# Kernel optimization log

Measured on AMD Instinct MI355X. Metric: run time of the kernel, lower is better.

## Reference

```python
import jax, jax.numpy as jnp
import numpy as np

B, S, E, H = 8, 1025, 1408, 16
D = E // H  # 88 head_dim


def setup_inputs() -> dict:
    key = jax.random.key(0)
    ks = jax.random.split(key, 12)
    w_scale = 0.02
    hidden_states = jax.random.normal(ks[0], (B, S, E), dtype=jnp.float32)
    ang = jax.random.uniform(ks[1], (S, D // 2), dtype=jnp.float32) * (2.0 * np.pi)
    freqs_cos = jnp.cos(ang)
    freqs_sin = jnp.sin(ang)
    Wq = jax.random.normal(ks[2], (E, E), dtype=jnp.float32) * w_scale
    bq = jax.random.normal(ks[3], (E,), dtype=jnp.float32) * w_scale
    Wk = jax.random.normal(ks[4], (E, E), dtype=jnp.float32) * w_scale
    bk = jax.random.normal(ks[5], (E,), dtype=jnp.float32) * w_scale
    Wv = jax.random.normal(ks[6], (E, E), dtype=jnp.float32) * w_scale
    bv = jax.random.normal(ks[7], (E,), dtype=jnp.float32) * w_scale
    Wo = jax.random.normal(ks[8], (E, E), dtype=jnp.float32) * w_scale
    bo = jax.random.normal(ks[9], (E,), dtype=jnp.float32) * w_scale
    return {"hidden_states": hidden_states, "freqs_cos": freqs_cos, "freqs_sin": freqs_sin,
            "Wq": Wq, "bq": bq, "Wk": Wk, "bk": bk, "Wv": Wv, "bv": bv, "Wo": Wo, "bo": bo}


def _apply_rope(x, cos, sin):
    # x: (B,S,H,D); interpret last dim as D/2 complex pairs (real, imag)
    xr = x[..., 0::2]  # (B,S,H,D/2) -- pairs laid out interleaved after reshape(..., -1, 2)
    xi = x[..., 1::2]
    c = cos[None, :, None, :]  # (1,S,1,D/2)
    s = sin[None, :, None, :]
    or_ = xr * c - xi * s
    oi_ = xr * s + xi * c
    # interleave back: (..., D/2, 2) -> (..., D)
    return jnp.stack([or_, oi_], axis=-1).reshape(x.shape)


def reference(hidden_states, freqs_cos, freqs_sin, Wq, bq, Wk, bk, Wv, bv, Wo, bo):
    b, s, e = hidden_states.shape
    h, d = H, D
    q = (hidden_states @ Wq.T + bq).reshape(b, s, h, d)
    k = (hidden_states @ Wk.T + bk).reshape(b, s, h, d)
    v = (hidden_states @ Wv.T + bv).reshape(b, s, h, d)
    q = _apply_rope(q, freqs_cos, freqs_sin)
    k = _apply_rope(k, freqs_cos, freqs_sin)
    scale = d ** (-0.5)
    # (B,H,S,S) attention scores; no mask, non-causal, dropout=0 (eval)
    scores = jnp.einsum("bshd,bthd->bhst", q, k) * scale
    w = jax.nn.softmax(scores, axis=-1)
    out = jnp.einsum("bhst,bthd->bshd", w, v).reshape(b, s, e)
    return out @ Wo.T + bo
```

## Files before the change

kernel.cpp:

```cpp
#include <hip/hip_runtime.h>
#include <stdint.h>
#include <stddef.h>

#define Bsz 8
#define Ssz 1025
#define Esz 1408
#define Hsz 16
#define Dsz 88
#define Msz (Bsz * Ssz)
#define HALF_E (Esz / 2)
#define HALF_D (Dsz / 2)
#define SPAD 1088
#define QSC 0.15379182f

typedef __attribute__((ext_vector_type(8))) short short8;
typedef __attribute__((ext_vector_type(4))) float f32x4;

__device__ __forceinline__ unsigned short f2bf(float f) {
  union { float f; unsigned u; } v; v.f = f;
  unsigned r = v.u + 0x7fffu + ((v.u >> 16) & 1u);
  return (unsigned short)(r >> 16);
}
__device__ __forceinline__ unsigned fbits(float f) {
  union { float f; unsigned u; } v; v.f = f; return v.u;
}
__device__ __forceinline__ float fexp2(float x) {
#if __has_builtin(__builtin_amdgcn_exp2f)
  return __builtin_amdgcn_exp2f(x);
#else
  return __expf(x * 0.6931471805599453f);
#endif
}

__global__ void cast_kernel(const float* __restrict__ in, unsigned short* __restrict__ out, int n4) {
  int i = blockIdx.x * blockDim.x + threadIdx.x;
  if (i >= n4) return;
  float4 v = ((const float4*)in)[i];
  uint2 o;
  o.x = (unsigned)f2bf(v.x) | ((unsigned)f2bf(v.y) << 16);
  o.y = (unsigned)f2bf(v.z) | ((unsigned)f2bf(v.w) << 16);
  ((uint2*)out)[i] = o;
}

__global__ void cast4_kernel(const float* __restrict__ a, const float* __restrict__ b,
                             const float* __restrict__ c, const float* __restrict__ d,
                             unsigned short* __restrict__ out, int n4each) {
  int i = blockIdx.x * blockDim.x + threadIdx.x;
  if (i >= 4 * n4each) return;
  int sel = i / n4each, off = i - sel * n4each;
  const float* src = (sel == 0) ? a : (sel == 1) ? b : (sel == 2) ? c : d;
  float4 v = ((const float4*)src)[off];
  uint2 o;
  o.x = (unsigned)f2bf(v.x) | ((unsigned)f2bf(v.y) << 16);
  o.y = (unsigned)f2bf(v.z) | ((unsigned)f2bf(v.w) << 16);
  ((uint2*)(out))[i] = o;
}

template <int OUT_BF16>
__global__ __launch_bounds__(256)
void gemm_bt(const unsigned short* __restrict__ A, const unsigned short* __restrict__ Bw,
             const float* __restrict__ bias, void* __restrict__ Cout,
             int M, int N, int K) {
  __shared__ __attribute__((aligned(16))) unsigned short sA[128 * 32];
  __shared__ __attribute__((aligned(16))) unsigned short sB[128 * 32];
  const int tid  = threadIdx.x;
  const int wave = tid >> 6;
  const int lane = tid & 63;
  const int m0 = blockIdx.y * 128;
  const int n0 = blockIdx.x * 128;
  const int wm = (wave >> 1) * 64;
  const int wn = (wave & 1) * 64;
  const int l15 = lane & 15;
  const int q8  = (lane >> 4) * 8;
  const int lr  = lane >> 2;
  const int lc  = (lane & 3) * 8;

  const f32x4 z4 = {0.f, 0.f, 0.f, 0.f};
  f32x4 acc[4][4];
  for (int i = 0; i < 4; i++)
    for (int j = 0; j < 4; j++) acc[i][j] = z4;

  for (int k0 = 0; k0 < K; k0 += 32) {
    __syncthreads();
#pragma unroll
    for (int c = 0; c < 2; c++) {
      int row = wave * 32 + c * 16;
      int gm = m0 + row + lr; if (gm > M - 1) gm = M - 1;
      const unsigned short* gpa = A + (size_t)gm * K + (k0 + lc);
      __builtin_amdgcn_global_load_lds(
          (__attribute__((address_space(1))) void*)gpa,
          (__attribute__((address_space(3))) void*)(&sA[row * 32]),
          16, 0, 0);
      int gn = n0 + row + lr;
      const unsigned short* gpb = Bw + (size_t)gn * K + (k0 + lc);
      __builtin_amdgcn_global_load_lds(
          (__attribute__((address_space(1))) void*)gpb,
          (__attribute__((address_space(3))) void*)(&sB[row * 32]),
          16, 0, 0);
    }
    __syncthreads();

    short8 af[4], bfv[4];
#pragma unroll
    for (int i = 0; i < 4; i++) af[i]  = *(const short8*)&sA[(wm + i * 16 + l15) * 32 + q8];
#pragma unroll
    for (int j = 0; j < 4; j++) bfv[j] = *(const short8*)&sB[(wn + j * 16 + l15) * 32 + q8];
#pragma unroll
    for (int i = 0; i < 4; i++)
#pragma unroll
      for (int j = 0; j < 4; j++)
        acc[i][j] = __builtin_amdgcn_mfma_f32_16x16x32_bf16(af[i], bfv[j], acc[i][j], 0, 0, 0);
  }

#pragma unroll
  for (int i = 0; i < 4; i++) {
#pragma unroll
    for (int j = 0; j < 4; j++) {
      int n = n0 + wn + j * 16 + l15;
      float bias_n = bias[n];
#pragma unroll
      for (int r = 0; r < 4; r++) {
        int m = m0 + wm + i * 16 + (lane >> 4) * 4 + r;
        if (m < M) {
          float val = acc[i][j][r] + bias_n;
          if (OUT_BF16) ((unsigned short*)Cout)[(size_t)m * N + n] = f2bf(val);
          else          ((float*)Cout)[(size_t)m * N + n] = val;
        }
      }
    }
  }
}

__global__ __launch_bounds__(256)
void gemm_qkv(const unsigned short* __restrict__ A, const unsigned short* __restrict__ W,
              const float* __restrict__ bq, const float* __restrict__ bk,
              const float* __restrict__ bv,
              const float* __restrict__ cosp, const float* __restrict__ sinp,
              unsigned short* __restrict__ qkv, int M, int K) {
  __shared__ __attribute__((aligned(16))) unsigned short sA[128 * 32];
  __shared__ __attribute__((aligned(16))) unsigned short sB[128 * 32];
  const int tid  = threadIdx.x;
  const int wave = tid >> 6;
  const int lane = tid & 63;
  const int m0 = blockIdx.y * 128;
  const int n0 = blockIdx.x * 128;
  const int wm = (wave >> 1) * 64;
  const int wn = (wave & 1) * 64;
  const int l15 = lane & 15;
  const int q8  = (lane >> 4) * 8;
  const int quad4 = (lane >> 4) * 4;
  const int lr  = lane >> 2;
  const int lc  = (lane & 3) * 8;

  const f32x4 z4 = {0.f, 0.f, 0.f, 0.f};
  f32x4 acc[4][4];
  for (int i = 0; i < 4; i++)
    for (int j = 0; j < 4; j++) acc[i][j] = z4;

  for (int k0 = 0; k0 < K; k0 += 32) {
    __syncthreads();
#pragma unroll
    for (int c = 0; c < 2; c++) {
      int row = wave * 32 + c * 16;
      int gm = m0 + row + lr; if (gm > M - 1) gm = M - 1;
      const unsigned short* gpa = A + (size_t)gm * K + (k0 + lc);
      __builtin_amdgcn_global_load_lds(
          (__attribute__((address_space(1))) void*)gpa,
          (__attribute__((address_space(3))) void*)(&sA[row * 32]),
          16, 0, 0);
      int gn = n0 + row + lr;
      const unsigned short* gpb = W + (size_t)gn * K + (k0 + lc);
      __builtin_amdgcn_global_load_lds(
          (__attribute__((address_space(1))) void*)gpb,
          (__attribute__((address_space(3))) void*)(&sB[row * 32]),
          16, 0, 0);
    }
    __syncthreads();

    short8 af[4], bfv[4];
#pragma unroll
    for (int i = 0; i < 4; i++) af[i]  = *(const short8*)&sA[(wm + i * 16 + l15) * 32 + q8];
#pragma unroll
    for (int j = 0; j < 4; j++) bfv[j] = *(const short8*)&sB[(wn + j * 16 + l15) * 32 + q8];
#pragma unroll
    for (int i = 0; i < 4; i++)
#pragma unroll
      for (int j = 0; j < 4; j++)
        acc[i][j] = __builtin_amdgcn_mfma_f32_16x16x32_bf16(af[i], bfv[j], acc[i][j], 0, 0, 0);
  }

  const int sel   = blockIdx.x / 11;
  const int nloc0 = (blockIdx.x % 11) * 128;
  const float* bias = (sel == 0) ? bq : (sel == 1) ? bk : bv;
  unsigned short* outb = qkv + (size_t)sel * ((size_t)Msz * Esz);

#pragma unroll
  for (int i = 0; i < 4; i++) {
#pragma unroll
    for (int j = 0; j < 4; j++) {
      int nl = nloc0 + wn + j * 16 + l15;
      float bias_n = bias[nl];
      int dd = nl % Dsz;
      int jrot = dd >> 1;
      bool isEven = (nl & 1) == 0;
#pragma unroll
      for (int r = 0; r < 4; r++) {
        int m = m0 + wm + i * 16 + quad4 + r;
        float val = acc[i][j][r] + bias_n;
        if (sel < 2) {
          float pv = __shfl_xor(val, 1, 64);
          int sp = m - (m / Ssz) * Ssz;
          float c  = cosp[sp * HALF_D + jrot];
          float sn = sinp[sp * HALF_D + jrot];
          val = isEven ? (val * c - pv * sn) : (pv * sn + val * c);
        }
        if (sel == 0) val *= QSC;
        if (m < M) outb[(size_t)m * Esz + nl] = f2bf(val);
      }
    }
  }
}

__global__ __launch_bounds__(256)
void vtrans_kernel(const unsigned short* __restrict__ vb, unsigned short* __restrict__ vt) {
  __shared__ unsigned short sT[64 * 89 + 8];
  const int tid = threadIdx.x;
  const int st = blockIdx.x, hh = blockIdx.y, bb = blockIdx.z;
  const short8 z8 = {0, 0, 0, 0, 0, 0, 0, 0};
  const unsigned short* src = vb + (size_t)(bb * Ssz) * Esz + hh * Dsz;
#pragma unroll
  for (int it = 0; it < 3; it++) {
    int g = it * 256 + tid;
    if (g < 704) {
      int r = g / 11, gc = g - r * 11;
      int s = st * 64 + r;
      short8 v = z8;
      if (s < Ssz) v = *(const short8*)(src + (size_t)s * Esz + gc * 8);
#pragma unroll
      for (int i = 0; i < 8; i++) sT[r * 89 + gc * 8 + i] = v[i];
    }
  }
  __syncthreads();
  unsigned short* dst = vt + (size_t)((bb * Hsz + hh) * Dsz) * SPAD + st * 64;
#pragma unroll
  for (int it = 0; it < 3; it++) {
    int g = it * 256 + tid;
    if (g < 704) {
      int d = g >> 3, sc = g & 7;
      short8 v;
#pragma unroll
      for (int i = 0; i < 8; i++) v[i] = sT[(sc * 8 + i) * 89 + d];
      *(short8*)(dst + (size_t)d * SPAD + sc * 8) = v;
    }
  }
}

__global__ __launch_bounds__(256)
void attn_kernel(const unsigned short* __restrict__ qp, const unsigned short* __restrict__ kp,
                 const unsigned short* __restrict__ vt, unsigned short* __restrict__ op) {
  __shared__ __attribute__((aligned(16))) unsigned short sK[64 * 88 + 16];
  __shared__ __attribute__((aligned(16))) unsigned short sVT[96 * 72];
  __shared__ __attribute__((aligned(16))) unsigned short sP[64 * 72];
  const int tid  = threadIdx.x;
  const int wave = tid >> 6, lane = tid & 63;
  const int qt = blockIdx.x, hh = blockIdx.y, bb = blockIdx.z;
  const int l15 = lane & 15, quad = lane >> 4;
  const int quad4 = quad * 4;
  const short8 z8 = {0, 0, 0, 0, 0, 0, 0, 0};

  short8 qf[2][3];
#pragma unroll
  for (int st2 = 0; st2 < 2; st2++) {
    int s = qt * 128 + st2 * 64 + wave * 16 + l15; if (s > Ssz - 1) s = Ssz - 1;
    const unsigned short* qrow = qp + (size_t)(bb * Ssz + s) * Esz + hh * Dsz;
#pragma unroll
    for (int ks = 0; ks < 3; ks++) {
      short8 v = z8;
      if (!(ks == 2 && quad == 3)) v = *(const short8*)(qrow + ks * 32 + quad * 8);
      qf[st2][ks] = v;
    }
  }

  const unsigned short* kbase  = kp + (size_t)(bb * Ssz) * Esz + hh * Dsz;
  const unsigned short* vtbase = vt + (size_t)((bb * Hsz + hh) * Dsz) * SPAD;
  unsigned* sPu = (unsigned*)sP;

  float m_i[2] = {-1e30f, -1e30f}, l_i[2] = {0.f, 0.f};
  const f32x4 z4 = {0.f, 0.f, 0.f, 0.f};
  f32x4 o_acc[2][6];
#pragma unroll
  for (int st2 = 0; st2 < 2; st2++)
#pragma unroll
    for (int jd = 0; jd < 6; jd++) o_acc[st2][jd] = z4;

  for (int kt = 0; kt < 17; kt++) {
    __syncthreads();
    for (int c = wave; c < 11; c += 4) {
      int g = c * 64 + lane;
      int r = g / 11, gc = g - r * 11;
      int t = kt * 64 + r; if (t > Ssz - 1) t = Ssz - 1;
      const unsigned short* srcp = kbase + (size_t)t * Esz + gc * 8;
      __builtin_amdgcn_global_load_lds(
          (__attribute__((address_space(1))) void*)srcp,
          (__attribute__((address_space(3))) void*)(&sK[c * 512]),
          16, 0, 0);
    }
#pragma unroll
    for (int it = 0; it < 3; it++) {
      int g = it * 256 + tid;
      if (g < 704) {
        int d = g >> 3, sc2 = g & 7;
        short8 v = *(const short8*)(vtbase + (size_t)d * SPAD + kt * 64 + sc2 * 8);
        *(short8*)&sVT[d * 72 + sc2 * 8] = v;
      }
    }
    __syncthreads();

#pragma unroll
    for (int st2 = 0; st2 < 2; st2++) {
      f32x4 stv[4];
#pragma unroll
      for (int j = 0; j < 4; j++) stv[j] = z4;
#pragma unroll
      for (int ks = 0; ks < 3; ks++) {
#pragma unroll
        for (int j = 0; j < 4; j++) {
          short8 bk8 = *(const short8*)&sK[(j * 16 + l15) * 88 + ks * 32 + quad * 8];
          stv[j] = __builtin_amdgcn_mfma_f32_16x16x32_bf16(bk8, qf[st2][ks], stv[j], 0, 0, 0);
        }
      }

      if (kt == 16) {
#pragma unroll
        for (int j = 0; j < 4; j++)
#pragma unroll
          for (int r = 0; r < 4; r++)
            if (j != 0 || r != 0) stv[j][r] = -1e30f;
        if (quad != 0) stv[0][0] = -1e30f;
      }

      float rmax = stv[0][0];
#pragma unroll
      for (int j = 0; j < 4; j++)
#pragma unroll
        for (int r = 0; r < 4; r++) rmax = fmaxf(rmax, stv[j][r]);
      rmax = fmaxf(rmax, __shfl_xor(rmax, 16, 64));
      rmax = fmaxf(rmax, __shfl_xor(rmax, 32, 64));

      float mnew = fmaxf(m_i[st2], rmax);
      float alpha = fexp2(m_i[st2] - mnew);
      m_i[st2] = mnew;

      float rsum = 0.f;
#pragma unroll
      for (int j = 0; j < 4; j++) {
        float p0 = fexp2(stv[j][0] - mnew);
        float p1 = fexp2(stv[j][1] - mnew);
        float p2 = fexp2(stv[j][2] - mnew);
        float p3 = fexp2(stv[j][3] - mnew);
        rsum += (p0 + p1) + (p2 + p3);
        unsigned w0 = __builtin_amdgcn_perm(fbits(p1) + 0x8000u, fbits(p0) + 0x8000u, 0x07060302u);
        unsigned w1 = __builtin_amdgcn_perm(fbits(p3) + 0x8000u, fbits(p2) + 0x8000u, 0x07060302u);
        int base = (wave * 16 + l15) * 36 + j * 8 + quad * 2;
        sPu[base]     = w0;
        sPu[base + 1] = w1;
      }
      rsum += __shfl_xor(rsum, 16, 64);
      rsum += __shfl_xor(rsum, 32, 64);
      l_i[st2] = l_i[st2] * alpha + rsum;

      float ar[4];
#pragma unroll
      for (int r = 0; r < 4; r++) ar[r] = __shfl(alpha, quad4 + r, 64);
#pragma unroll
      for (int jd = 0; jd < 6; jd++)
#pragma unroll
        for (int r = 0; r < 4; r++) o_acc[st2][jd][r] *= ar[r];

#pragma unroll
      for (int ks2 = 0; ks2 < 2; ks2++) {
        short8 ap = *(const short8*)&sP[(wave * 16 + l15) * 72 + ks2 * 32 + quad * 8];
#pragma unroll
        for (int jd = 0; jd < 6; jd++) {
          short8 bv8 = *(const short8*)&sVT[(jd * 16 + l15) * 72 + ks2 * 32 + quad * 8];
          o_acc[st2][jd] = __builtin_amdgcn_mfma_f32_16x16x32_bf16(ap, bv8, o_acc[st2][jd], 0, 0, 0);
        }
      }
    }
  }

#pragma unroll
  for (int st2 = 0; st2 < 2; st2++) {
    float lr4[4];
#pragma unroll
    for (int r = 0; r < 4; r++) lr4[r] = __shfl(l_i[st2], quad4 + r, 64);
#pragma unroll
    for (int jd = 0; jd < 6; jd++) {
      int d = jd * 16 + l15;
#pragma unroll
      for (int r = 0; r < 4; r++) {
        int s = qt * 128 + st2 * 64 + wave * 16 + quad4 + r;
        if (s < Ssz && d < Dsz) {
          float val = o_acc[st2][jd][r] / lr4[r];
          op[((size_t)(bb * Ssz + s)) * Esz + hh * Dsz + d] = f2bf(val);
        }
      }
    }
  }
}

extern "C" void kernel_launch(void* const* d_in, const int* in_sizes, int n_in,
                              void* d_out, int out_size, void* d_ws, size_t ws_size,
                              hipStream_t stream) {
  const float* hs = (const float*)d_in[0];
  const float* fc = (const float*)d_in[1];
  const float* fs = (const float*)d_in[2];
  const float* Wq = (const float*)d_in[3];
  const float* bq = (const float*)d_in[4];
  const float* Wk = (const float*)d_in[5];
  const float* bk = (const float*)d_in[6];
  const float* Wv = (const float*)d_in[7];
  const float* bv = (const float*)d_in[8];
  const float* Wo = (const float*)d_in[9];
  const float* bo = (const float*)d_in[10];
  float* out = (float*)d_out;

  const size_t ME = (size_t)Msz * Esz;
  const size_t EE = (size_t)Esz * Esz;
  unsigned short* hsb = (unsigned short*)d_ws;
  unsigned short* wqb = hsb + ME;
  unsigned short* wkb = wqb + EE;
  unsigned short* wvb = wkb + EE;
  unsigned short* wob = wvb + EE;
  unsigned short* qb  = wob + EE;
  unsigned short* kb  = qb  + ME;
  unsigned short* vb  = kb  + ME;
  unsigned short* vtb = hsb;
  unsigned short* aob = vb;

  int nh4 = (int)(ME / 4);
  int nw4 = (int)(EE / 4);
  cast_kernel<<<(nh4 + 255) / 256, 256, 0, stream>>>(hs, hsb, nh4);
  cast4_kernel<<<(4 * nw4 + 255) / 256, 256, 0, stream>>>(Wq, Wk, Wv, Wo, wqb, nw4);

  dim3 gq(33, (Msz + 127) / 128);
  gemm_qkv<<<gq, 256, 0, stream>>>(hsb, wqb, bq, bk, bv, fc, fs, qb, Msz, Esz);

  vtrans_kernel<<<dim3(17, Hsz, Bsz), 256, 0, stream>>>(vb, vtb);

  attn_kernel<<<dim3(9, Hsz, Bsz), 256, 0, stream>>>(qb, kb, vtb, aob);

  dim3 gg(Esz / 128, (Msz + 127) / 128);
  gemm_bt<0><<<gg, 256, 0, stream>>>(aob, wob, bo, out, Msz, Esz, Esz);
}
```

Baseline: 580.4 us.

## Double-buffer K tiles and prefetch V in attention, halve queries per block

The attention kernel now double-buffers the K tile in shared memory and prefetches the next V^T tile into registers, so the global loads for tile kt+1 overlap the compute on tile kt. Each block now handles 64 query rows instead of 128, and the grid grows from 9 to 17 query tiles. This gives more blocks and fewer registers per thread, at the cost of loading K/V twice as often overall and using more LDS per block.

```diff
diff --git a/kernel.cpp b/kernel.cpp
--- a/kernel.cpp
+++ b/kernel.cpp
@@ -258,7 +258,7 @@
 __global__ __launch_bounds__(256)
 void attn_kernel(const unsigned short* __restrict__ qp, const unsigned short* __restrict__ kp,
                  const unsigned short* __restrict__ vt, unsigned short* __restrict__ op) {
-  __shared__ __attribute__((aligned(16))) unsigned short sK[64 * 88 + 16];
+  __shared__ __attribute__((aligned(16))) unsigned short sK[2][64 * 88];
   __shared__ __attribute__((aligned(16))) unsigned short sVT[96 * 72];
   __shared__ __attribute__((aligned(16))) unsigned short sP[64 * 72];
   const int tid  = threadIdx.x;
@@ -268,16 +268,15 @@
   const int quad4 = quad * 4;
   const short8 z8 = {0, 0, 0, 0, 0, 0, 0, 0};
 
-  short8 qf[2][3];
-#pragma unroll
-  for (int st2 = 0; st2 < 2; st2++) {
-    int s = qt * 128 + st2 * 64 + wave * 16 + l15; if (s > Ssz - 1) s = Ssz - 1;
+  short8 qf[3];
+  {
+    int s = qt * 64 + wave * 16 + l15; if (s > Ssz - 1) s = Ssz - 1;
     const unsigned short* qrow = qp + (size_t)(bb * Ssz + s) * Esz + hh * Dsz;
 #pragma unroll
     for (int ks = 0; ks < 3; ks++) {
       short8 v = z8;
       if (!(ks == 2 && quad == 3)) v = *(const short8*)(qrow + ks * 32 + quad * 8);
-      qf[st2][ks] = v;
+      qf[ks] = v;
     }
   }
 
@@ -285,125 +284,161 @@
   const unsigned short* vtbase = vt + (size_t)((bb * Hsz + hh) * Dsz) * SPAD;
   unsigned* sPu = (unsigned*)sP;
 
-  float m_i[2] = {-1e30f, -1e30f}, l_i[2] = {0.f, 0.f};
-  const f32x4 z4 = {0.f, 0.f, 0.f, 0.f};
-  f32x4 o_acc[2][6];
-#pragma unroll
-  for (int st2 = 0; st2 < 2; st2++)
-#pragma unroll
-    for (int jd = 0; jd < 6; jd++) o_acc[st2][jd] = z4;
-
-  for (int kt = 0; kt < 17; kt++) {
-    __syncthreads();
-    for (int c = wave; c < 11; c += 4) {
+  const int kc_r[3]  = {(0 * 64 + lane) / 11, (4 * 64 + lane) / 11, (8 * 64 + lane) / 11};
+
+#pragma unroll
+  for (int ci = 0; ci < 3; ci++) {
+    int c = wave + ci * 4;
+    if (c < 11) {
       int g = c * 64 + lane;
       int r = g / 11, gc = g - r * 11;
-      int t = kt * 64 + r; if (t > Ssz - 1) t = Ssz - 1;
+      int t = r;
       const unsigned short* srcp = kbase + (size_t)t * Esz + gc * 8;
       __builtin_amdgcn_global_load_lds(
           (__attribute__((address_space(1))) void*)srcp,
-          (__attribute__((address_space(3))) void*)(&sK[c * 512]),
+          (__attribute__((address_space(3))) void*)(&sK[0][c * 512]),
           16, 0, 0);
     }
+  }
+  short8 vreg[3];
+#pragma unroll
+  for (int it = 0; it < 3; it++) {
+    int g = it * 256 + tid;
+    if (g < 704) {
+      int d = g >> 3, sc2 = g & 7;
+      vreg[it] = *(const short8*)(vtbase + (size_t)d * SPAD + 0 * 64 + sc2 * 8);
+    }
+  }
+
+  float m_i = -1e30f, l_i = 0.f;
+  const f32x4 z4 = {0.f, 0.f, 0.f, 0.f};
+  f32x4 o_acc[6];
+#pragma unroll
+  for (int jd = 0; jd < 6; jd++) o_acc[jd] = z4;
+
+  int cur = 0;
+  for (int kt = 0; kt < 17; kt++) {
+    __syncthreads();
 #pragma unroll
     for (int it = 0; it < 3; it++) {
       int g = it * 256 + tid;
       if (g < 704) {
         int d = g >> 3, sc2 = g & 7;
-        short8 v = *(const short8*)(vtbase + (size_t)d * SPAD + kt * 64 + sc2 * 8);
-        *(short8*)&sVT[d * 72 + sc2 * 8] = v;
-      }
-    }
-    __syncthreads();
-
-#pragma unroll
-    for (int st2 = 0; st2 < 2; st2++) {
-      f32x4 stv[4];
-#pragma unroll
-      for (int j = 0; j < 4; j++) stv[j] = z4;
-#pragma unroll
-      for (int ks = 0; ks < 3; ks++) {
-#pragma unroll
-        for (int j = 0; j < 4; j++) {
-          short8 bk8 = *(const short8*)&sK[(j * 16 + l15) * 88 + ks * 32 + quad * 8];
-          stv[j] = __builtin_amdgcn_mfma_f32_16x16x32_bf16(bk8, qf[st2][ks], stv[j], 0, 0, 0);
+        *(short8*)&sVT[d * 72 + sc2 * 8] = vreg[it];
+      }
+    }
+    __syncthreads();
+
+    if (kt < 16) {
+      int ktn = kt + 1;
+#pragma unroll
+      for (int ci = 0; ci < 3; ci++) {
+        int c = wave + ci * 4;
+        if (c < 11) {
+          int g = c * 64 + lane;
+          int r = g / 11, gc = g - r * 11;
+          int t = ktn * 64 + r; if (t > Ssz - 1) t = Ssz - 1;
+          const unsigned short* srcp = kbase + (size_t)t * Esz + gc * 8;
+          __builtin_amdgcn_global_load_lds(
+              (__attribute__((address_space(1))) void*)srcp,
+              (__attribute__((address_space(3))) void*)(&sK[cur ^ 1][c * 512]),
+              16, 0, 0);
         }
       }
-
-      if (kt == 16) {
-#pragma unroll
-        for (int j = 0; j < 4; j++)
-#pragma unroll
-          for (int r = 0; r < 4; r++)
-            if (j != 0 || r != 0) stv[j][r] = -1e30f;
-        if (quad != 0) stv[0][0] = -1e30f;
-      }
-
-      float rmax = stv[0][0];
+#pragma unroll
+      for (int it = 0; it < 3; it++) {
+        int g = it * 256 + tid;
+        if (g < 704) {
+          int d = g >> 3, sc2 = g & 7;
+          vreg[it] = *(const short8*)(vtbase + (size_t)d * SPAD + ktn * 64 + sc2 * 8);
+        }
+      }
+    }
+
+    const unsigned short* sKc = sK[cur];
+    f32x4 stv[4];
+#pragma unroll
+    for (int j = 0; j < 4; j++) stv[j] = z4;
+#pragma unroll
+    for (int ks = 0; ks < 3; ks++) {
+#pragma unroll
+      for (int j = 0; j < 4; j++) {
+        short8 bk8 = *(const short8*)&sKc[(j * 16 + l15) * 88 + ks * 32 + quad * 8];
+        stv[j] = __builtin_amdgcn_mfma_f32_16x16x32_bf16(bk8, qf[ks], stv[j], 0, 0, 0);
+      }
+    }
+
+    if (kt == 16) {
 #pragma unroll
       for (int j = 0; j < 4; j++)
 #pragma unroll
-        for (int r = 0; r < 4; r++) rmax = fmaxf(rmax, stv[j][r]);
-      rmax = fmaxf(rmax, __shfl_xor(rmax, 16, 64));
-      rmax = fmaxf(rmax, __shfl_xor(rmax, 32, 64));
-
-      float mnew = fmaxf(m_i[st2], rmax);
-      float alpha = fexp2(m_i[st2] - mnew);
-      m_i[st2] = mnew;
-
-      float rsum = 0.f;
-#pragma unroll
-      for (int j = 0; j < 4; j++) {
-        float p0 = fexp2(stv[j][0] - mnew);
-        float p1 = fexp2(stv[j][1] - mnew);
-        float p2 = fexp2(stv[j][2] - mnew);
-        float p3 = fexp2(stv[j][3] - mnew);
-        rsum += (p0 + p1) + (p2 + p3);
-        unsigned w0 = __builtin_amdgcn_perm(fbits(p1) + 0x8000u, fbits(p0) + 0x8000u, 0x07060302u);
-        unsigned w1 = __builtin_amdgcn_perm(fbits(p3) + 0x8000u, fbits(p2) + 0x8000u, 0x07060302u);
-        int base = (wave * 16 + l15) * 36 + j * 8 + quad * 2;
-        sPu[base]     = w0;
-        sPu[base + 1] = w1;
-      }
-      rsum += __shfl_xor(rsum, 16, 64);
-      rsum += __shfl_xor(rsum, 32, 64);
-      l_i[st2] = l_i[st2] * alpha + rsum;
-
-      float ar[4];
-#pragma unroll
-      for (int r = 0; r < 4; r++) ar[r] = __shfl(alpha, quad4 + r, 64);
-#pragma unroll
-      for (int jd = 0; jd < 6; jd++)
-#pragma unroll
-        for (int r = 0; r < 4; r++) o_acc[st2][jd][r] *= ar[r];
-
-#pragma unroll
-      for (int ks2 = 0; ks2 < 2; ks2++) {
-        short8 ap = *(const short8*)&sP[(wave * 16 + l15) * 72 + ks2 * 32 + quad * 8];
-#pragma unroll
-        for (int jd = 0; jd < 6; jd++) {
-          short8 bv8 = *(const short8*)&sVT[(jd * 16 + l15) * 72 + ks2 * 32 + quad * 8];
-          o_acc[st2][jd] = __builtin_amdgcn_mfma_f32_16x16x32_bf16(ap, bv8, o_acc[st2][jd], 0, 0, 0);
-        }
-      }
-    }
-  }
-
-#pragma unroll
-  for (int st2 = 0; st2 < 2; st2++) {
-    float lr4[4];
-#pragma unroll
-    for (int r = 0; r < 4; r++) lr4[r] = __shfl(l_i[st2], quad4 + r, 64);
-#pragma unroll
-    for (int jd = 0; jd < 6; jd++) {
-      int d = jd * 16 + l15;
-#pragma unroll
-      for (int r = 0; r < 4; r++) {
-        int s = qt * 128 + st2 * 64 + wave * 16 + quad4 + r;
-        if (s < Ssz && d < Dsz) {
-          float val = o_acc[st2][jd][r] / lr4[r];
-          op[((size_t)(bb * Ssz + s)) * Esz + hh * Dsz + d] = f2bf(val);
-        }
+        for (int r = 0; r < 4; r++)
+          if (j != 0 || r != 0) stv[j][r] = -1e30f;
+      if (quad != 0) stv[0][0] = -1e30f;
+    }
+
+    float rmax = stv[0][0];
+#pragma unroll
+    for (int j = 0; j < 4; j++)
+#pragma unroll
+      for (int r = 0; r < 4; r++) rmax = fmaxf(rmax, stv[j][r]);
+    rmax = fmaxf(rmax, __shfl_xor(rmax, 16, 64));
+    rmax = fmaxf(rmax, __shfl_xor(rmax, 32, 64));
+
+    float mnew = fmaxf(m_i, rmax);
+    float alpha = fexp2(m_i - mnew);
+    m_i = mnew;
+
+    float rsum = 0.f;
+#pragma unroll
+    for (int j = 0; j < 4; j++) {
+      float p0 = fexp2(stv[j][0] - mnew);
+      float p1 = fexp2(stv[j][1] - mnew);
+      float p2 = fexp2(stv[j][2] - mnew);
+      float p3 = fexp2(stv[j][3] - mnew);
+      rsum += (p0 + p1) + (p2 + p3);
+      unsigned w0 = __builtin_amdgcn_perm(fbits(p1) + 0x8000u, fbits(p0) + 0x8000u, 0x07060302u);
+      unsigned w1 = __builtin_amdgcn_perm(fbits(p3) + 0x8000u, fbits(p2) + 0x8000u, 0x07060302u);
+      int base = (wave * 16 + l15) * 36 + j * 8 + quad * 2;
+      sPu[base]     = w0;
+      sPu[base + 1] = w1;
+    }
+    rsum += __shfl_xor(rsum, 16, 64);
+    rsum += __shfl_xor(rsum, 32, 64);
+    l_i = l_i * alpha + rsum;
+
+    float ar[4];
+#pragma unroll
+    for (int r = 0; r < 4; r++) ar[r] = __shfl(alpha, quad4 + r, 64);
+#pragma unroll
+    for (int jd = 0; jd < 6; jd++)
+#pragma unroll
+      for (int r = 0; r < 4; r++) o_acc[jd][r] *= ar[r];
+
+#pragma unroll
+    for (int ks2 = 0; ks2 < 2; ks2++) {
+      short8 ap = *(const short8*)&sP[(wave * 16 + l15) * 72 + ks2 * 32 + quad * 8];
+#pragma unroll
+      for (int jd = 0; jd < 6; jd++) {
+        short8 bv8 = *(const short8*)&sVT[(jd * 16 + l15) * 72 + ks2 * 32 + quad * 8];
+        o_acc[jd] = __builtin_amdgcn_mfma_f32_16x16x32_bf16(ap, bv8, o_acc[jd], 0, 0, 0);
+      }
+    }
+    cur ^= 1;
+  }
+
+  float lr4[4];
+#pragma unroll
+  for (int r = 0; r < 4; r++) lr4[r] = __shfl(l_i, quad4 + r, 64);
+#pragma unroll
+  for (int jd = 0; jd < 6; jd++) {
+    int d = jd * 16 + l15;
+#pragma unroll
+    for (int r = 0; r < 4; r++) {
+      int s = qt * 64 + wave * 16 + quad4 + r;
+      if (s < Ssz && d < Dsz) {
+        float val = o_acc[jd][r] / lr4[r];
+        op[((size_t)(bb * Ssz + s)) * Esz + hh * Dsz + d] = f2bf(val);
       }
     }
   }
@@ -448,7 +483,7 @@
 
   vtrans_kernel<<<dim3(17, Hsz, Bsz), 256, 0, stream>>>(vb, vtb);
 
-  attn_kernel<<<dim3(9, Hsz, Bsz), 256, 0, stream>>>(qb, kb, vtb, aob);
+  attn_kernel<<<dim3(17, Hsz, Bsz), 256, 0, stream>>>(qb, kb, vtb, aob);
 
   dim3 gg(Esz / 128, (Msz + 127) / 128);
   gemm_bt<0><<<gg, 256, 0, stream>>>(aob, wob, bo, out, Msz, Esz, Esz);
```

New measurement: 511.7 us. 11.8% less time.
